# Performance work log

Hardware: AMD Instinct MI355X
Metric: run time of the kernel (lower is better)

## Reference

```python
import jax, jax.numpy as jnp
import numpy as np

B, N, F_IN = 4, 8000, 3          # batch, electrons per event, (x,y,z) features
HID, S, T = 128, 1024, 1024      # MLP hidden, n_sensors, waveform_ticks
INV_SQRT_2PI = 0.3989422804


def _mlp(x, W1, b1, W2, b2):
    h = jax.nn.relu(x @ W1 + b1)
    return h @ W2 + b2


def setup_inputs() -> dict:
    key = jax.random.key(0)
    ks = jax.random.split(key, 12)
    simulator_input = jax.random.normal(ks[0], (B, N, F_IN), dtype=jnp.float32)
    # z positions in tick units, spread across the waveform
    z_positions = jax.random.uniform(ks[1], (B, N), dtype=jnp.float32) * (T - 1)
    mask = jnp.ones((B, N, 1), dtype=jnp.float32)
    s1 = 1.0 / np.sqrt(F_IN)
    s2 = 1.0 / np.sqrt(HID)
    Wp1 = jax.random.normal(ks[2], (F_IN, HID), dtype=jnp.float32) * s1
    bp1 = jnp.zeros((HID,), dtype=jnp.float32)
    Wp2 = jax.random.normal(ks[3], (HID, S), dtype=jnp.float32) * s2
    bp2 = jnp.zeros((S,), dtype=jnp.float32)
    Wa1 = jax.random.normal(ks[4], (F_IN, HID), dtype=jnp.float32) * s1
    ba1 = jnp.zeros((HID,), dtype=jnp.float32)
    Wa2 = jax.random.normal(ks[5], (HID, S), dtype=jnp.float32) * s2
    ba2 = jnp.zeros((S,), dtype=jnp.float32)
    nn_bin_sigma = 5.0 * jnp.ones((1,), dtype=jnp.float32)  # self.variable init
    return dict(simulator_input=simulator_input, z_positions=z_positions, mask=mask,
                Wp1=Wp1, bp1=bp1, Wp2=Wp2, bp2=bp2,
                Wa1=Wa1, ba1=ba1, Wa2=Wa2, ba2=ba2,
                nn_bin_sigma=nn_bin_sigma)


def reference(simulator_input, z_positions, mask,
              Wp1, bp1, Wp2, bp2, Wa1, ba1, Wa2, ba2, nn_bin_sigma):
    # sensor response per electron: sigmoid(prob MLP) * amp MLP * mask  -> [B,N,S]
    sensor_probs = jax.nn.sigmoid(_mlp(simulator_input, Wp1, bp1, Wp2, bp2))
    el_light_amp = _mlp(simulator_input, Wa1, ba1, Wa2, ba2)
    response_of_sensors = el_light_amp * sensor_probs * mask

    # Gaussian binning kernel over waveform ticks: [B,N,T]
    ticks = jnp.arange(T, dtype=simulator_input.dtype)          # linspace(0, T-1, T)
    sigma = nn_bin_sigma[0]
    diff = ticks[None, None, :] - z_positions[:, :, None]
    exp_values = jnp.exp(-(diff ** 2) / (2.0 * sigma ** 2)) * (INV_SQRT_2PI / jnp.sqrt(sigma ** 2))

    # per-batch waveforms = sensor_response.T @ exp_values -> [B,S,T]; then sum over batch
    waveforms = jnp.einsum('bns,bnt->st', response_of_sensors, exp_values)
    return waveforms  # [S, T]
```

## Files before the change

kernel.cpp:

```cpp
#include <hip/hip_runtime.h>


#define BN_E   32000
#define NBLK   125
#define HIDW   128
#define S_DIM  1024
#define T_DIM  1024
#define NBKT   16
#define KSPL   4
#define MAXPAD (BN_E + NBKT * 31)
#define MAXCG  ((MAXPAD + 31) / 32)
#define INV_SQRT_2PI 0.3989422804f

typedef __attribute__((ext_vector_type(8))) unsigned short u16x8;
typedef __attribute__((ext_vector_type(8))) __bf16         bf16x8;
typedef __attribute__((ext_vector_type(4))) float          f32x4;

static __device__ __forceinline__ unsigned short f2bf(float f) {
    union { float f; unsigned int u; } v; v.f = f;
    unsigned int r = v.u + 0x7FFFu + ((v.u >> 16) & 1u);
    return (unsigned short)(r >> 16);
}

static __device__ __forceinline__ f32x4 mfma16(u16x8 a, u16x8 b, f32x4 c) {
    return __builtin_amdgcn_mfma_f32_16x16x32_bf16(
        __builtin_bit_cast(bf16x8, a), __builtin_bit_cast(bf16x8, b), c, 0, 0, 0);
}

static __device__ __forceinline__ int bucket_of(float z) {
    int b = (int)floorf((z - 31.f) * (1.f / 64.f));
    return min(max(b, 0), NBKT - 1);
}

__global__ __launch_bounds__(256) void k_count(const float* __restrict__ z,
                                               int* __restrict__ bc,
                                               float* __restrict__ out) {
    int bx = blockIdx.x;
    if (bx >= NBLK) {
        int idx = (bx - NBLK) * 256 + threadIdx.x;
        ((f32x4*)out)[idx] = (f32x4){0.f, 0.f, 0.f, 0.f};
        return;
    }
    __shared__ int h[NBKT];
    if (threadIdx.x < NBKT) h[threadIdx.x] = 0;
    __syncthreads();
    int e = bx * 256 + threadIdx.x;
    atomicAdd(&h[bucket_of(z[e])], 1);
    __syncthreads();
    if (threadIdx.x < NBKT) bc[bx * NBKT + threadIdx.x] = h[threadIdx.x];
}

__global__ __launch_bounds__(256) void k_fillscan(const float* __restrict__ z,
                                                  const int* __restrict__ bc,
                                                  int* __restrict__ meta,
                                                  int* __restrict__ list) {
    __shared__ int part[16][16];
    __shared__ int segoff[16][16];
    __shared__ int cntL[NBKT], pstartL[NBKT], baseL[NBKT], h[NBKT];
    int t = threadIdx.x, b = t & 15, seg = t >> 4;
    int v[8]; int sum = 0;
#pragma unroll
    for (int i = 0; i < 8; ++i) {
        int blk = seg * 8 + i;
        v[i] = (blk < NBLK) ? bc[blk * NBKT + b] : 0;
        sum += v[i];
    }
    part[seg][b] = sum;
    if (t < NBKT) h[t] = 0;
    __syncthreads();
    if (t < NBKT) {
        int run = 0;
        for (int s = 0; s < 16; ++s) { segoff[s][t] = run; run += part[s][t]; }
        cntL[t] = run;
    }
    __syncthreads();
    if (t == 0) {
        int s = 0;
        for (int i = 0; i < NBKT; ++i) {
            pstartL[i] = s;
            s += ((cntL[i] + 31) >> 5) << 5;
        }
        if (blockIdx.x == 0) {
            for (int i = 0; i < NBKT; ++i) { meta[i] = cntL[i]; meta[32 + i] = pstartL[i]; }
            meta[48] = s;
        }
    }
    __syncthreads();
    if (t < NBKT) {
        int me = blockIdx.x;
        int run = segoff[me >> 3][t];
        for (int k = 0; k < (me & 7); ++k)
            run += bc[((me >> 3) * 8 + k) * NBKT + t];
        baseL[t] = pstartL[t] + run;
    }
    __syncthreads();
    int e = blockIdx.x * 256 + t;
    int b2 = bucket_of(z[e]);
    int r = atomicAdd(&h[b2], 1);
    list[baseL[b2] + r] = e;
}

__global__ __launch_bounds__(256) void k_prep(
    const float* __restrict__ x, const float* __restrict__ zg,
    const float* __restrict__ maskg, const float* __restrict__ sigp,
    const float* __restrict__ Wp1, const float* __restrict__ bp1,
    const float* __restrict__ Wa1, const float* __restrict__ ba1,
    const float* __restrict__ Wp2, const float* __restrict__ Wa2,
    const int* __restrict__ meta, const int* __restrict__ list,
    unsigned short* __restrict__ HpS, unsigned short* __restrict__ HaS,
    unsigned short* __restrict__ GT,
    unsigned short* __restrict__ WfP, unsigned short* __restrict__ WfA) {
    int bx = blockIdx.x;
    if (bx < MAXCG) {
        int pos0 = bx * 32;
        if (pos0 >= meta[48]) return;
        int b = 15;
        while (meta[32 + b] > pos0) --b;
        int tb = b * 64, cnt = meta[b], pstart = meta[32 + b];
        int tid = threadIdx.x;

        __shared__ float W1L[1024];
        __shared__ float zzL[32], cmL[32];
        if (tid < 96)                        ((float4*)W1L)[tid]              = ((const float4*)Wp1)[tid];
        else if (tid < 128)                  ((float4*)(W1L + 384))[tid - 96] = ((const float4*)bp1)[tid - 96];
        else if (tid < 224)                  ((float4*)(W1L + 512))[tid - 128]= ((const float4*)Wa1)[tid - 128];
        else                                 ((float4*)(W1L + 896))[tid - 224]= ((const float4*)ba1)[tid - 224];
        if (tid < 32) {
            int pos = pos0 + tid;
            bool real = (pos - pstart) < cnt;
            int ev = real ? list[pos] : 0;
            float sigma = sigp[0];
            zzL[tid] = real ? zg[ev] : 0.f;
            cmL[tid] = real ? (INV_SQRT_2PI / sigma) * maskg[ev] : 0.f;
        }
        __syncthreads();

        {
            int e_l = tid >> 3, part = tid & 7;
            int pos = pos0 + e_l;
            bool real = (pos - pstart) < cnt;
            int ev = real ? list[pos] : 0;
            float x0 = 0.f, x1 = 0.f, x2 = 0.f;
            if (real) { x0 = x[ev * 3]; x1 = x[ev * 3 + 1]; x2 = x[ev * 3 + 2]; }
            unsigned short hp[16], ha[16];
#pragma unroll
            for (int i = 0; i < 16; ++i) {
                int j = part * 16 + i;
                float hv = x0 * W1L[j] + x1 * W1L[128 + j] + x2 * W1L[256 + j] + W1L[384 + j];
                float av = x0 * W1L[512 + j] + x1 * W1L[640 + j] + x2 * W1L[768 + j] + W1L[896 + j];
                hp[i] = real ? f2bf(fmaxf(hv, 0.f)) : (unsigned short)0;
                ha[i] = real ? f2bf(fmaxf(av, 0.f)) : (unsigned short)0;
            }
#pragma unroll
            for (int h2 = 0; h2 < 2; ++h2) {
                int k0 = part * 16 + h2 * 8;
                int u = ((k0 >> 5) * 4 + ((k0 >> 3) & 3)) * 32 + e_l;
                *(uint4*)&HpS[(size_t)bx * 4096 + u * 8] = ((uint4*)hp)[h2];
                *(uint4*)&HaS[(size_t)bx * 4096 + u * 8] = ((uint4*)ha)[h2];
            }
        }

        {
            float sigma = sigp[0];
            float nis2 = -1.f / (2.f * sigma * sigma);
#pragma unroll
            for (int uu = 0; uu < 2; ++uu) {
                int u = tid * 2 + uu;
                int n8 = u >> 6, q = (u >> 4) & 3, c = u & 15;
                float tt = (float)(tb + n8 * 16 + c);
                unsigned short g8[8];
#pragma unroll
                for (int j = 0; j < 8; ++j) {
                    int e = q * 8 + j;
                    float d = tt - zzL[e];
                    g8[j] = f2bf(cmL[e] * __expf(d * d * nis2));
                }
                *(uint4*)&GT[(size_t)bx * 4096 + u * 8] = *(uint4*)g8;
            }
        }
    } else {
        int bid = bx - MAXCG;
        const float* src = (bid & 64) ? Wa2 : Wp2;
        unsigned short* dst = (bid & 64) ? WfA : WfP;
        int rem = bid & 63;
        int kq = rem >> 2;
        int s  = (rem & 3) * 256 + threadIdx.x;
        int ks = kq >> 2, q = kq & 3;
        unsigned short fr[8];
#pragma unroll
        for (int j = 0; j < 8; ++j)
            fr[j] = f2bf(src[(ks * 32 + q * 8 + j) * S_DIM + s]);
        ((u16x8*)dst)[kq * S_DIM + s] = *(u16x8*)fr;
    }
}

__global__ __launch_bounds__(256, 4) void k_main(
    const unsigned short* __restrict__ HpS, const unsigned short* __restrict__ HaS,
    const unsigned short* __restrict__ WfP, const unsigned short* __restrict__ WfA,
    const float* __restrict__ bp2, const float* __restrict__ ba2,
    const int* __restrict__ meta, const unsigned short* __restrict__ GT,
    float* __restrict__ out) {

    const int bk     = blockIdx.x / KSPL;
    const int kspl   = blockIdx.x % KSPL;
    const int s0     = blockIdx.y * 64;
    const int tb     = bk * 64;
    const int cnt    = meta[bk];
    const int pstart = meta[32 + bk];
    const int nch    = (cnt + 31) >> 5;
    const int per    = (nch + KSPL - 1) / KSPL;
    const int c0     = kspl * per;
    const int c1     = min(nch, c0 + per);
    if (c0 >= c1) return;

    const int tid = threadIdx.x;
    const int w = tid >> 6, l = tid & 63, q = l >> 4, c = l & 15;

    __shared__ __align__(16) uint4 HpL[512];
    __shared__ __align__(16) uint4 HaL[512];
    __shared__ __align__(16) unsigned short RspL[64 * 40];

    const u16x8* WfPv = (const u16x8*)WfP;
    const u16x8* WfAv = (const u16x8*)WfA;
    const int sg = s0 + w * 16 + c;
    u16x8 wP[4], wA[4];
#pragma unroll
    for (int ks = 0; ks < 4; ++ks) {
        wP[ks] = WfPv[(ks * 4 + q) * S_DIM + sg];
        wA[ks] = WfAv[(ks * 4 + q) * S_DIM + sg];
    }
    const float bp2v = bp2[sg];
    const float ba2v = ba2[sg];

    const f32x4 z4 = { 0.f, 0.f, 0.f, 0.f };
    f32x4 acc2[8];
#pragma unroll
    for (int n8 = 0; n8 < 8; ++n8) acc2[n8] = z4;

    const uint4* Hp4 = (const uint4*)HpS;
    const uint4* Ha4 = (const uint4*)HaS;
    const int cgBase = pstart >> 5;
    const u16x8* StHp = (const u16x8*)HpL;
    const u16x8* StHa = (const u16x8*)HaL;

    size_t cb = (size_t)(cgBase + c0) * 512;
    uint4 p0 = Hp4[cb + tid], p1 = Hp4[cb + 256 + tid];
    uint4 a0 = Ha4[cb + tid], a1 = Ha4[cb + 256 + tid];

    for (int ci = c0; ci < c1; ++ci) {
        __syncthreads();
        HpL[tid] = p0; HpL[256 + tid] = p1;
        HaL[tid] = a0; HaL[256 + tid] = a1;
        __syncthreads();

        int nc = min(ci + 1, c1 - 1);
        cb = (size_t)(cgBase + nc) * 512;
        p0 = Hp4[cb + tid]; p1 = Hp4[cb + 256 + tid];
        a0 = Ha4[cb + tid]; a1 = Ha4[cb + 256 + tid];

        const unsigned short* gt = GT + (size_t)(cgBase + ci) * 4096;
        u16x8 bfr[8];
#pragma unroll
        for (int n8 = 0; n8 < 8; ++n8)
            bfr[n8] = *(const u16x8*)&gt[((n8 * 4 + q) * 16 + c) * 8];

        f32x4 aP[2], aA[2];
#pragma unroll
        for (int m = 0; m < 2; ++m) { aP[m] = z4; aA[m] = z4; }
#pragma unroll
        for (int ks = 0; ks < 4; ++ks) {
            u16x8 hp0 = StHp[(ks * 4 + q) * 32 + c];
            u16x8 hp1 = StHp[(ks * 4 + q) * 32 + c + 16];
            u16x8 ha0 = StHa[(ks * 4 + q) * 32 + c];
            u16x8 ha1 = StHa[(ks * 4 + q) * 32 + c + 16];
            aP[0] = mfma16(hp0, wP[ks], aP[0]);
            aP[1] = mfma16(hp1, wP[ks], aP[1]);
            aA[0] = mfma16(ha0, wA[ks], aA[0]);
            aA[1] = mfma16(ha1, wA[ks], aA[1]);
        }

#pragma unroll
        for (int m = 0; m < 2; ++m) {
            f32x4 p = aP[m], a = aA[m];
            unsigned long long pk = 0;
#pragma unroll
            for (int r = 0; r < 4; ++r) {
                float pr = p[r] + bp2v;
                float ar = a[r] + ba2v;
                float sg2 = __builtin_amdgcn_rcpf(1.f + __expf(-pr));
                pk |= (unsigned long long)f2bf(sg2 * ar) << (16 * r);
            }
            int sl = w * 16 + c;
            int e0 = m * 16 + q * 4;
            *(unsigned long long*)&RspL[sl * 40 + e0] = pk;
        }

        u16x8 afr = *(const u16x8*)&RspL[(w * 16 + c) * 40 + q * 8];
#pragma unroll
        for (int n8 = 0; n8 < 8; ++n8)
            acc2[n8] = mfma16(afr, bfr[n8], acc2[n8]);
    }

#pragma unroll
    for (int n8 = 0; n8 < 8; ++n8) {
        int t = tb + n8 * 16 + c;
        if (t < T_DIM) {
            int srow = s0 + w * 16 + q * 4;
#pragma unroll
            for (int r = 0; r < 4; ++r)
                atomicAdd(&out[(srow + r) * T_DIM + t], acc2[n8][r]);
        }
    }
}


extern "C" void kernel_launch(void* const* d_in, const int* in_sizes, int n_in,
                              void* d_out, int out_size, void* d_ws, size_t ws_size,
                              hipStream_t stream) {
    const float* x    = (const float*)d_in[0];
    const float* zp   = (const float*)d_in[1];
    const float* mask = (const float*)d_in[2];
    const float* Wp1  = (const float*)d_in[3];
    const float* bp1  = (const float*)d_in[4];
    const float* Wp2  = (const float*)d_in[5];
    const float* bp2  = (const float*)d_in[6];
    const float* Wa1  = (const float*)d_in[7];
    const float* ba1  = (const float*)d_in[8];
    const float* Wa2  = (const float*)d_in[9];
    const float* ba2  = (const float*)d_in[10];
    const float* sig  = (const float*)d_in[11];

    char* ws = (char*)d_ws;
    unsigned short* HpS  = (unsigned short*)(ws);
    unsigned short* HaS  = (unsigned short*)(ws + 8323072);
    unsigned short* WfP  = (unsigned short*)(ws + 16646144);
    unsigned short* WfA  = (unsigned short*)(ws + 16908288);
    int*            meta = (int*)(ws + 17170432);
    int*            list = (int*)(ws + 17170688);
    int*            bc   = (int*)(ws + 17300736);
    unsigned short* GT   = (unsigned short*)(ws + 17308736);

    k_count<<<NBLK + 1024, 256, 0, stream>>>(zp, bc, (float*)d_out);
    k_fillscan<<<NBLK, 256, 0, stream>>>(zp, bc, meta, list);
    k_prep<<<MAXCG + 128, 256, 0, stream>>>(x, zp, mask, sig,
                                            Wp1, bp1, Wa1, ba1, Wp2, Wa2,
                                            meta, list, HpS, HaS, GT, WfP, WfA);
    k_main<<<dim3(NBKT * KSPL, 16, 1), 256, 0, stream>>>(
        HpS, HaS, WfP, WfA, bp2, ba2, meta, GT, (float*)d_out);
}
```

Before: 152.6 us.

## Widen k_main sensor tile, double-buffer hidden staging, coalesce k_prep stores

k_main now runs 512-thread blocks covering 128 sensors instead of 64, so each block reads a chunk's Gaussian tile and hidden activations once for twice as many sensors. The grid's y dimension halves accordingly. Hidden-activation staging in LDS becomes double-buffered, dropping one __syncthreads per chunk iteration. In k_prep, the bucket metadata is cached in shared memory and threads are remapped so hidden-activation stores to global memory are coalesced. The trade-offs are higher per-block LDS use, larger blocks, and fewer blocks available to fill the GPU.

```diff
diff --git a/kernel.cpp b/kernel.cpp
--- a/kernel.cpp
+++ b/kernel.cpp
@@ -112,19 +112,24 @@
     unsigned short* __restrict__ WfP, unsigned short* __restrict__ WfA) {
     int bx = blockIdx.x;
     if (bx < MAXCG) {
-        int pos0 = bx * 32;
-        if (pos0 >= meta[48]) return;
-        int b = 15;
-        while (meta[32 + b] > pos0) --b;
-        int tb = b * 64, cnt = meta[b], pstart = meta[32 + b];
         int tid = threadIdx.x;
 
         __shared__ float W1L[1024];
         __shared__ float zzL[32], cmL[32];
+        __shared__ int metaL[33];
+        if (tid < 33) metaL[tid] = meta[tid < 16 ? tid : (tid < 32 ? tid + 16 : 48)];
         if (tid < 96)                        ((float4*)W1L)[tid]              = ((const float4*)Wp1)[tid];
         else if (tid < 128)                  ((float4*)(W1L + 384))[tid - 96] = ((const float4*)bp1)[tid - 96];
         else if (tid < 224)                  ((float4*)(W1L + 512))[tid - 128]= ((const float4*)Wa1)[tid - 128];
         else                                 ((float4*)(W1L + 896))[tid - 224]= ((const float4*)ba1)[tid - 224];
+        __syncthreads();
+
+        int pos0 = bx * 32;
+        if (pos0 >= metaL[32]) return;
+        int b = 15;
+        while (metaL[16 + b] > pos0) --b;
+        int tb = b * 64, cnt = metaL[b], pstart = metaL[16 + b];
+
         if (tid < 32) {
             int pos = pos0 + tid;
             bool real = (pos - pstart) < cnt;
@@ -133,10 +138,9 @@
             zzL[tid] = real ? zg[ev] : 0.f;
             cmL[tid] = real ? (INV_SQRT_2PI / sigma) * maskg[ev] : 0.f;
         }
-        __syncthreads();
 
         {
-            int e_l = tid >> 3, part = tid & 7;
+            int e_l = tid & 31, part = tid >> 5;
             int pos = pos0 + e_l;
             bool real = (pos - pstart) < cnt;
             int ev = real ? list[pos] : 0;
@@ -153,12 +157,12 @@
             }
 #pragma unroll
             for (int h2 = 0; h2 < 2; ++h2) {
-                int k0 = part * 16 + h2 * 8;
-                int u = ((k0 >> 5) * 4 + ((k0 >> 3) & 3)) * 32 + e_l;
+                int u = (2 * part + h2) * 32 + e_l;
                 *(uint4*)&HpS[(size_t)bx * 4096 + u * 8] = ((uint4*)hp)[h2];
                 *(uint4*)&HaS[(size_t)bx * 4096 + u * 8] = ((uint4*)ha)[h2];
             }
         }
+        __syncthreads();
 
         {
             float sigma = sigp[0];
@@ -194,7 +198,7 @@
     }
 }
 
-__global__ __launch_bounds__(256, 4) void k_main(
+__global__ __launch_bounds__(512, 4) void k_main(
     const unsigned short* __restrict__ HpS, const unsigned short* __restrict__ HaS,
     const unsigned short* __restrict__ WfP, const unsigned short* __restrict__ WfA,
     const float* __restrict__ bp2, const float* __restrict__ ba2,
@@ -203,7 +207,7 @@
 
     const int bk     = blockIdx.x / KSPL;
     const int kspl   = blockIdx.x % KSPL;
-    const int s0     = blockIdx.y * 64;
+    const int s0     = blockIdx.y * 128;
     const int tb     = bk * 64;
     const int cnt    = meta[bk];
     const int pstart = meta[32 + bk];
@@ -216,9 +220,9 @@
     const int tid = threadIdx.x;
     const int w = tid >> 6, l = tid & 63, q = l >> 4, c = l & 15;
 
-    __shared__ __align__(16) uint4 HpL[512];
-    __shared__ __align__(16) uint4 HaL[512];
-    __shared__ __align__(16) unsigned short RspL[64 * 40];
+    __shared__ __align__(16) uint4 HpL[1024];
+    __shared__ __align__(16) uint4 HaL[1024];
+    __shared__ __align__(16) unsigned short RspL[128 * 40];
 
     const u16x8* WfPv = (const u16x8*)WfP;
     const u16x8* WfAv = (const u16x8*)WfA;
@@ -240,23 +244,21 @@
     const uint4* Hp4 = (const uint4*)HpS;
     const uint4* Ha4 = (const uint4*)HaS;
     const int cgBase = pstart >> 5;
-    const u16x8* StHp = (const u16x8*)HpL;
-    const u16x8* StHa = (const u16x8*)HaL;
 
     size_t cb = (size_t)(cgBase + c0) * 512;
-    uint4 p0 = Hp4[cb + tid], p1 = Hp4[cb + 256 + tid];
-    uint4 a0 = Ha4[cb + tid], a1 = Ha4[cb + 256 + tid];
+    uint4 p = Hp4[cb + tid];
+    uint4 a = Ha4[cb + tid];
 
     for (int ci = c0; ci < c1; ++ci) {
-        __syncthreads();
-        HpL[tid] = p0; HpL[256 + tid] = p1;
-        HaL[tid] = a0; HaL[256 + tid] = a1;
-        __syncthreads();
+        const int buf = ((ci - c0) & 1) << 9;
+        HpL[buf + tid] = p;
+        HaL[buf + tid] = a;
 
         int nc = min(ci + 1, c1 - 1);
         cb = (size_t)(cgBase + nc) * 512;
-        p0 = Hp4[cb + tid]; p1 = Hp4[cb + 256 + tid];
-        a0 = Ha4[cb + tid]; a1 = Ha4[cb + 256 + tid];
+        p = Hp4[cb + tid];
+        a = Ha4[cb + tid];
+        __syncthreads();
 
         const unsigned short* gt = GT + (size_t)(cgBase + ci) * 4096;
         u16x8 bfr[8];
@@ -264,9 +266,10 @@
         for (int n8 = 0; n8 < 8; ++n8)
             bfr[n8] = *(const u16x8*)&gt[((n8 * 4 + q) * 16 + c) * 8];
 
+        const u16x8* StHp = (const u16x8*)(HpL + buf);
+        const u16x8* StHa = (const u16x8*)(HaL + buf);
         f32x4 aP[2], aA[2];
-#pragma unroll
-        for (int m = 0; m < 2; ++m) { aP[m] = z4; aA[m] = z4; }
+        aP[0] = z4; aP[1] = z4; aA[0] = z4; aA[1] = z4;
 #pragma unroll
         for (int ks = 0; ks < 4; ++ks) {
             u16x8 hp0 = StHp[(ks * 4 + q) * 32 + c];
@@ -281,18 +284,16 @@
 
 #pragma unroll
         for (int m = 0; m < 2; ++m) {
-            f32x4 p = aP[m], a = aA[m];
+            f32x4 pp = aP[m], aa = aA[m];
             unsigned long long pk = 0;
 #pragma unroll
             for (int r = 0; r < 4; ++r) {
-                float pr = p[r] + bp2v;
-                float ar = a[r] + ba2v;
+                float pr = pp[r] + bp2v;
+                float ar = aa[r] + ba2v;
                 float sg2 = __builtin_amdgcn_rcpf(1.f + __expf(-pr));
                 pk |= (unsigned long long)f2bf(sg2 * ar) << (16 * r);
             }
-            int sl = w * 16 + c;
-            int e0 = m * 16 + q * 4;
-            *(unsigned long long*)&RspL[sl * 40 + e0] = pk;
+            *(unsigned long long*)&RspL[(w * 16 + c) * 40 + m * 16 + q * 4] = pk;
         }
 
         u16x8 afr = *(const u16x8*)&RspL[(w * 16 + c) * 40 + q * 8];
@@ -345,6 +346,6 @@
     k_prep<<<MAXCG + 128, 256, 0, stream>>>(x, zp, mask, sig,
                                             Wp1, bp1, Wa1, ba1, Wp2, Wa2,
                                             meta, list, HpS, HaS, GT, WfP, WfA);
-    k_main<<<dim3(NBKT * KSPL, 16, 1), 256, 0, stream>>>(
+    k_main<<<dim3(NBKT * KSPL, 8, 1), 512, 0, stream>>>(
         HpS, HaS, WfP, WfA, bp2, ba2, meta, GT, (float*)d_out);
 }
```

Result: faster. 148.7 us (-2.5%).
